# Kernel optimization log

Measured on AMD Instinct MI355X. Metric: run time of the kernel, lower is better.

Reference implementation:

```python
import jax, jax.numpy as jnp
import numpy as np

N = 1024   # state dimension
L = 16384  # sequence length


def setup_inputs() -> dict:
    key = jax.random.key(0)
    k_u, k_a, k_b, k_c = jax.random.split(key, 4)
    u = jax.random.normal(k_u, (L,), dtype=jnp.float32)
    # lecun_normal: std = 1/sqrt(fan_in). Shift A by -I so the discretized
    # transition matrix Ab has spectral radius < 1 (otherwise Ab^L overflows).
    A = jax.random.normal(k_a, (N, N), dtype=jnp.float32) / np.sqrt(N) - jnp.eye(N, dtype=jnp.float32)
    B = jax.random.normal(k_b, (N, 1), dtype=jnp.float32) / np.sqrt(1.0)
    C = jax.random.normal(k_c, (1, N), dtype=jnp.float32) / np.sqrt(N)
    log_step = jnp.full((1, 1), np.log(0.01), dtype=jnp.float32)
    return {"u": u, "A": A, "B": B, "C": C, "log_step": log_step}


def reference(u, A, B, C, log_step):
    # --- discretize (bilinear / Tustin transform) ---
    step = jnp.exp(log_step)[0, 0]
    I = jnp.eye(A.shape[0], dtype=A.dtype)
    BL = jnp.linalg.inv(I - (step / 2.0) * A)
    Ab = BL @ (I + (step / 2.0) * A)     # (N, N)
    Bb = (step * BL) @ B                  # (N, 1)
    Cb = C                                # (1, N)

    # --- naive_kernel: K[l] = Cb @ Ab^l @ Bb, built as a scan recurrence ---
    def body(x, _):
        k_l = (Cb @ x)[0, 0]
        return Ab @ x, k_l

    _, K = jax.lax.scan(body, Bb, None, length=u.shape[0])  # (L,)

    # --- causal convolution: y[t] = sum_{l<=t} K[l] * u[t-l] ---
    y = jnp.convolve(u, K)[: u.shape[0]]
    return y
```

## Files before the change

kernel.cpp:

```cpp
#include <hip/hip_runtime.h>
#include <hip/hip_bf16.h>
#include <math.h>

#define N_DIM 1024
#define L_SEQ 16384

typedef unsigned short ushort_t;
typedef __bf16 bf16x8 __attribute__((ext_vector_type(8)));
typedef float f32x4 __attribute__((ext_vector_type(4)));

#define FW_F32 1
#define FW_SPLIT 2
#define FW_TSPLIT 4
#define FW_ADDD 8
#define FW_MKAB 16
#define FW_TPRE 32

#define AS1 __attribute__((address_space(1)))
#define AS3 __attribute__((address_space(3)))

__device__ __forceinline__ void split2(float v, ushort_t& h, ushort_t& m) {
  union { __bf16 b; ushort_t u; } c;
  __bf16 bh = (__bf16)v;
  float fh = (float)bh;
  c.b = bh; h = c.u;
  c.b = (__bf16)(v - fh); m = c.u;
}

__global__ __launch_bounds__(256) void k_scalesplit(const float* __restrict__ A,
    const float* __restrict__ ls, float* __restrict__ E,
    ushort_t* __restrict__ set) {
  const size_t NN = (size_t)N_DIM * N_DIM;
  float hs = 0.5f * expf(ls[0]);
  int t = threadIdx.x;
  int r0 = blockIdx.x * 64 + ((t >> 4) << 2);
  int c0 = blockIdx.y * 64 + ((t & 15) << 2);
  float v[4][4];
#pragma unroll
  for (int i = 0; i < 4; ++i) {
    float4 f = *(const float4*)&A[(size_t)(r0 + i) * N_DIM + c0];
    v[i][0] = hs * f.x; v[i][1] = hs * f.y; v[i][2] = hs * f.z; v[i][3] = hs * f.w;
    *(float4*)&E[(size_t)(r0 + i) * N_DIM + c0] =
        make_float4(v[i][0], v[i][1], v[i][2], v[i][3]);
  }
  ushort_t h[4][4], m[4][4];
#pragma unroll
  for (int i = 0; i < 4; ++i)
#pragma unroll
    for (int j = 0; j < 4; ++j) split2(v[i][j], h[i][j], m[i][j]);
#pragma unroll
  for (int i = 0; i < 4; ++i) {
    size_t o = (size_t)(r0 + i) * N_DIM + c0;
    *(ushort4*)&set[o] = make_ushort4(h[i][0], h[i][1], h[i][2], h[i][3]);
    *(ushort4*)&set[NN + o] = make_ushort4(m[i][0], m[i][1], m[i][2], m[i][3]);
  }
#pragma unroll
  for (int j = 0; j < 4; ++j) {
    size_t o = (size_t)(c0 + j) * N_DIM + r0;
    *(ushort4*)&set[2 * NN + o] = make_ushort4(h[0][j], h[1][j], h[2][j], h[3][j]);
    *(ushort4*)&set[3 * NN + o] = make_ushort4(m[0][j], m[1][j], m[2][j], m[3][j]);
  }
}

__global__ __launch_bounds__(256) void k_bbinit(ushort_t* __restrict__ VTset,
    ushort_t* __restrict__ Wset, const float* __restrict__ S,
    const float* __restrict__ B, const float* __restrict__ Cm,
    const float* __restrict__ ls) {
  const size_t KR = (size_t)128 * N_DIM;
  int bx = blockIdx.x;
  if (bx >= 256) {
    int i = (bx - 256) * 256 + threadIdx.x;
    ushort_t h, m; split2(Cm[i], h, m);
    Wset[i] = h; Wset[KR + i] = m;
    return;
  }
  int row = bx * 4 + (threadIdx.x >> 6);
  int lane = threadIdx.x & 63;
  const float* Sr = S + (size_t)row * N_DIM;
  float sum = 0.f;
  for (int k = lane; k < N_DIM; k += 64) sum += Sr[k] * B[k];
  for (int off = 32; off; off >>= 1) sum += __shfl_down(sum, off);
  if (lane == 0) {
    float step = expf(ls[0]);
    float bb = step * (B[row] + sum);
    ushort_t h, m; split2(bb, h, m);
    VTset[row] = h; VTset[KR + row] = m;
  }
}

__device__ __forceinline__ void skinny_q(
    ushort_t* lds, const ushort_t* __restrict__ SkB, ushort_t* __restrict__ Ka,
    int srcOff, int dstOff, int cnt, int id, int t) {
  const size_t NN = (size_t)N_DIM * N_DIM;
  const size_t KR = (size_t)128 * N_DIM;
  int rt = id >> 6, c16 = id & 63;
  if (rt * 16 >= cnt) return;
  const int lane = t & 63, w = t >> 6;
  const ushort_t* Ah = Ka;
  const ushort_t* Amm = Ka + KR;
  const ushort_t* Bh = SkB;
  const ushort_t* Bm = SkB + NN;

  auto stq = [&](int buf, int k0) {
    ushort_t* base = lds + buf * 2048;
    if (t < 128) {
      int pl = t >> 6, rem = t & 63, kc = rem >> 4, row = rem & 15;
      const ushort_t* src = (pl ? Amm : Ah) +
          (size_t)(srcOff + rt * 16 + row) * N_DIM + k0 + kc * 8;
      __builtin_amdgcn_global_load_lds((const AS1 void*)src,
                                       (AS3 void*)(base + t * 8), 16, 0, 0);
    } else {
      int t2 = t - 128;
      int pl = t2 >> 6, rem = t2 & 63, kc = rem >> 4, row = rem & 15;
      const ushort_t* src = (pl ? Bm : Bh) +
          (size_t)(c16 * 16 + row) * N_DIM + k0 + kc * 8;
      __builtin_amdgcn_global_load_lds((const AS1 void*)src,
                                       (AS3 void*)(base + 1024 + t2 * 8), 16, 0, 0);
    }
  };

  f32x4 acc = (f32x4){0.f, 0.f, 0.f, 0.f};
  const int lrow = lane & 15, kg = lane >> 4;

  stq(0, 0);
  stq(1, 32);
  for (int ks = 0; ks < 32; ++ks) {
    int cur = ks % 3;
    if (ks < 30) {
      stq((ks + 2) % 3, (ks + 2) * 32);
      asm volatile("s_waitcnt vmcnt(2)" ::: "memory");
    } else if (ks == 30) {
      asm volatile("s_waitcnt vmcnt(1)" ::: "memory");
    } else {
      asm volatile("s_waitcnt vmcnt(0)" ::: "memory");
    }
    __builtin_amdgcn_s_barrier();
    __builtin_amdgcn_sched_barrier(0);
    if (w == 0) {
      const ushort_t* b = lds + cur * 2048;
      bf16x8 a0 = *(const bf16x8*)&b[kg * 128 + lrow * 8];
      bf16x8 a1 = *(const bf16x8*)&b[512 + kg * 128 + lrow * 8];
      bf16x8 b0 = *(const bf16x8*)&b[1024 + kg * 128 + lrow * 8];
      bf16x8 b1 = *(const bf16x8*)&b[1536 + kg * 128 + lrow * 8];
      acc = __builtin_amdgcn_mfma_f32_16x16x32_bf16(a0, b0, acc, 0, 0, 0);
      acc = __builtin_amdgcn_mfma_f32_16x16x32_bf16(a0, b1, acc, 0, 0, 0);
      acc = __builtin_amdgcn_mfma_f32_16x16x32_bf16(a1, b0, acc, 0, 0, 0);
      acc = __builtin_amdgcn_mfma_f32_16x16x32_bf16(a1, b1, acc, 0, 0, 0);
    }
    if (ks < 31) __builtin_amdgcn_s_barrier();
  }

  if (w == 0) {
    int col = c16 * 16 + lrow;
#pragma unroll
    for (int j = 0; j < 4; ++j) {
      int irl = kg * 4 + j;
      if (rt * 16 + irl < cnt) {
        ushort_t h, m; split2(acc[j], h, m);
        Ka[(size_t)(dstOff + rt * 16 + irl) * N_DIM + col] = h;
        Ka[KR + (size_t)(dstOff + rt * 16 + irl) * N_DIM + col] = m;
      }
    }
  }
}

__global__ __launch_bounds__(256) void gemm4f(
    const ushort_t* __restrict__ Qa, const ushort_t* __restrict__ Qbt,
    const float* __restrict__ D, float* __restrict__ Cf,
    ushort_t* __restrict__ Oset, ushort_t* __restrict__ Oset2, int flags,
    const ushort_t* __restrict__ SkB, ushort_t* __restrict__ Ka,
    int srcOff, int dstOff, int cnt, int mode) {
  const size_t NN = (size_t)N_DIM * N_DIM;
  const size_t KR = (size_t)128 * N_DIM;
  __shared__ __align__(16) ushort_t lds[30720];
  int t = threadIdx.x;
  const int lane = t & 63, w = t >> 6;
  int id = (int)blockIdx.y * 16 + (int)blockIdx.x;

  if (mode == 2) {
    skinny_q(lds, SkB, Ka, srcOff, dstOff, cnt, id, t);
    return;
  }

  int m0 = blockIdx.x * 64, n0 = blockIdx.y * 64;
  int r = t & 63, kc = t >> 6;
  const ushort_t* gA[2] = {Qa, Qa + NN};
  const ushort_t* gB[2] = {Qbt, Qbt + NN};
  size_t aoff = (size_t)(m0 + r) * N_DIM + kc * 8;
  size_t boff = (size_t)(n0 + r) * N_DIM + kc * 8;

  int rt = id >> 6, c16 = id & 63;
  bool hasSk = (mode == 1) && (rt * 16 < cnt);
  const ushort_t* skAh = Ka;
  const ushort_t* skAm = Ka + KR;
  const ushort_t* skBh = SkB;
  const ushort_t* skBm = SkB ? SkB + NN : SkB;

  auto stage = [&](int buf, int k0) {
    ushort_t* dst = lds + buf * 8192;
#pragma unroll
    for (int L = 0; L < 2; ++L) {
      __builtin_amdgcn_global_load_lds(
          (const AS1 void*)(gA[L] + aoff + k0),
          (AS3 void*)(dst + L * 2048 + t * 8), 16, 0, 0);
      __builtin_amdgcn_global_load_lds(
          (const AS1 void*)(gB[L] + boff + k0),
          (AS3 void*)(dst + 4096 + L * 2048 + t * 8), 16, 0, 0);
    }
  };
  auto stq = [&](int buf, int k0) {
    ushort_t* base = lds + 24576 + buf * 2048;
    if (t < 128) {
      int pl = t >> 6, rem = t & 63, skc = rem >> 4, row = rem & 15;
      const ushort_t* src = (pl ? skAm : skAh) +
          (size_t)(srcOff + rt * 16 + row) * N_DIM + k0 + skc * 8;
      __builtin_amdgcn_global_load_lds((const AS1 void*)src,
                                       (AS3 void*)(base + t * 8), 16, 0, 0);
    } else {
      int t2 = t - 128;
      int pl = t2 >> 6, rem = t2 & 63, skc = rem >> 4, row = rem & 15;
      const ushort_t* src = (pl ? skBm : skBh) +
          (size_t)(c16 * 16 + row) * N_DIM + k0 + skc * 8;
      __builtin_amdgcn_global_load_lds((const AS1 void*)src,
                                       (AS3 void*)(base + 1024 + t2 * 8), 16, 0, 0);
    }
  };

  f32x4 acc[2][2];
#pragma unroll
  for (int i = 0; i < 2; ++i)
#pragma unroll
    for (int j = 0; j < 2; ++j) acc[i][j] = (f32x4){0.f, 0.f, 0.f, 0.f};
  f32x4 skacc = (f32x4){0.f, 0.f, 0.f, 0.f};

  const int wm = (w >> 1) * 32, wn = (w & 1) * 32;
  const int lrow = lane & 15, kg = lane >> 4;
  const int aIdx0 = kg * 512 + (wm + lrow) * 8;
  const int bIdx0 = 4096 + kg * 512 + (wn + lrow) * 8;

#pragma unroll
  for (int p = 0; p < 2; ++p) {
    stage(p, p * 32);
    if (hasSk) stq(p, p * 32);
  }
  for (int ks = 0; ks < 32; ++ks) {
    int cur = ks % 3;
    if (ks < 30) {
      stage((ks + 2) % 3, (ks + 2) * 32);
      if (hasSk) {
        stq((ks + 2) % 3, (ks + 2) * 32);
        asm volatile("s_waitcnt vmcnt(10)" ::: "memory");
      } else {
        asm volatile("s_waitcnt vmcnt(8)" ::: "memory");
      }
    } else if (ks == 30) {
      if (hasSk) asm volatile("s_waitcnt vmcnt(5)" ::: "memory");
      else       asm volatile("s_waitcnt vmcnt(4)" ::: "memory");
    } else {
      asm volatile("s_waitcnt vmcnt(0)" ::: "memory");
    }
    __builtin_amdgcn_s_barrier();
    __builtin_amdgcn_sched_barrier(0);
    const ushort_t* buf = lds + cur * 8192;
    bf16x8 a[2][2], b[2][2];
#pragma unroll
    for (int L = 0; L < 2; ++L) {
#pragma unroll
      for (int mi = 0; mi < 2; ++mi)
        a[L][mi] = *(const bf16x8*)&buf[L * 2048 + aIdx0 + mi * 128];
#pragma unroll
      for (int ni = 0; ni < 2; ++ni)
        b[L][ni] = *(const bf16x8*)&buf[bIdx0 + L * 2048 + ni * 128];
    }
#pragma unroll
    for (int mi = 0; mi < 2; ++mi)
#pragma unroll
      for (int ni = 0; ni < 2; ++ni) {
        f32x4 c = acc[mi][ni];
        c = __builtin_amdgcn_mfma_f32_16x16x32_bf16(a[0][mi], b[0][ni], c, 0, 0, 0);
        c = __builtin_amdgcn_mfma_f32_16x16x32_bf16(a[0][mi], b[1][ni], c, 0, 0, 0);
        c = __builtin_amdgcn_mfma_f32_16x16x32_bf16(a[1][mi], b[0][ni], c, 0, 0, 0);
        c = __builtin_amdgcn_mfma_f32_16x16x32_bf16(a[1][mi], b[1][ni], c, 0, 0, 0);
        acc[mi][ni] = c;
      }
    if (hasSk && w == 0) {
      const ushort_t* sb = lds + 24576 + cur * 2048;
      bf16x8 sa0 = *(const bf16x8*)&sb[kg * 128 + lrow * 8];
      bf16x8 sa1 = *(const bf16x8*)&sb[512 + kg * 128 + lrow * 8];
      bf16x8 sb0 = *(const bf16x8*)&sb[1024 + kg * 128 + lrow * 8];
      bf16x8 sb1 = *(const bf16x8*)&sb[1536 + kg * 128 + lrow * 8];
      skacc = __builtin_amdgcn_mfma_f32_16x16x32_bf16(sa0, sb0, skacc, 0, 0, 0);
      skacc = __builtin_amdgcn_mfma_f32_16x16x32_bf16(sa0, sb1, skacc, 0, 0, 0);
      skacc = __builtin_amdgcn_mfma_f32_16x16x32_bf16(sa1, sb0, skacc, 0, 0, 0);
      skacc = __builtin_amdgcn_mfma_f32_16x16x32_bf16(sa1, sb1, skacc, 0, 0, 0);
    }
    if (ks < 31) __builtin_amdgcn_s_barrier();
  }

#pragma unroll
  for (int mi = 0; mi < 2; ++mi)
#pragma unroll
    for (int ni = 0; ni < 2; ++ni) {
      int rowb = m0 + wm + mi * 16 + kg * 4;
      int col = n0 + wn + ni * 16 + lrow;
      float vv[4];
#pragma unroll
      for (int j = 0; j < 4; ++j) vv[j] = acc[mi][ni][j];
      if (flags & FW_TPRE) {
        ushort_t h[4], m[4];
#pragma unroll
        for (int j = 0; j < 4; ++j) split2(vv[j], h[j], m[j]);
        size_t o = (size_t)col * N_DIM + rowb;
        *(ushort4*)&Oset2[2 * NN + o] = make_ushort4(h[0], h[1], h[2], h[3]);
        *(ushort4*)&Oset2[3 * NN + o] = make_ushort4(m[0], m[1], m[2], m[3]);
      }
      if (flags & FW_ADDD) {
#pragma unroll
        for (int j = 0; j < 4; ++j) vv[j] += D[(size_t)(rowb + j) * N_DIM + col];
      }
      if (flags & FW_F32) {
#pragma unroll
        for (int j = 0; j < 4; ++j) Cf[(size_t)(rowb + j) * N_DIM + col] = vv[j];
      }
      if (flags & FW_MKAB) {
#pragma unroll
        for (int j = 0; j < 4; ++j)
          vv[j] = 2.0f * vv[j] + ((rowb + j) == col ? 1.0f : 0.0f);
      }
      if (flags & (FW_SPLIT | FW_TSPLIT)) {
        ushort_t h[4], m[4];
#pragma unroll
        for (int j = 0; j < 4; ++j) split2(vv[j], h[j], m[j]);
        if (flags & FW_SPLIT) {
#pragma unroll
          for (int j = 0; j < 4; ++j) {
            size_t o = (size_t)(rowb + j) * N_DIM + col;
            Oset[o] = h[j]; Oset[NN + o] = m[j];
          }
        }
        if (flags & FW_TSPLIT) {
          size_t o = (size_t)col * N_DIM + rowb;
          *(ushort4*)&Oset[2 * NN + o] = make_ushort4(h[0], h[1], h[2], h[3]);
          *(ushort4*)&Oset[3 * NN + o] = make_ushort4(m[0], m[1], m[2], m[3]);
        }
      }
    }

  if (hasSk && w == 0) {
    int col = c16 * 16 + lrow;
#pragma unroll
    for (int j = 0; j < 4; ++j) {
      int irl = kg * 4 + j;
      if (rt * 16 + irl < cnt) {
        ushort_t h, m; split2(skacc[j], h, m);
        Ka[(size_t)(dstOff + rt * 16 + irl) * N_DIM + col] = h;
        Ka[KR + (size_t)(dstOff + rt * 16 + irl) * N_DIM + col] = m;
      }
    }
  }
}

__global__ __launch_bounds__(256) void k_combine(
    const ushort_t* __restrict__ Wset, const ushort_t* __restrict__ Vset,
    float* __restrict__ Kv) {
  const size_t KR = (size_t)128 * N_DIM;
  __shared__ __align__(16) ushort_t lds[15360];
  int t = threadIdx.x;
  int rt = blockIdx.x, ct = blockIdx.y;
  const ushort_t* Ah = Wset;
  const ushort_t* Amm = Wset + KR;
  const ushort_t* Bh = Vset;
  const ushort_t* Bm = Vset + KR;
  const int lane = t & 63, w = t >> 6;
  const int lrow = lane & 15, kg = lane >> 4;

  auto stageS = [&](int buf, int k0) {
    ushort_t* base = lds + buf * 5120;
    if (t < 128) {
      int lvl = t >> 6, rem = t & 63, kcc = rem >> 4, i = rem & 15;
      const ushort_t* src =
          (lvl ? Amm : Ah) + (size_t)(rt * 16 + i) * N_DIM + k0 + kcc * 8;
      __builtin_amdgcn_global_load_lds((const AS1 void*)src,
                                       (AS3 void*)(base + t * 8), 16, 0, 0);
    }
#pragma unroll
    for (int it = 0; it < 2; ++it) {
      int t2 = t + it * 256;
      int lvl = t2 >> 8, rem = t2 & 255, kcc = rem >> 6, c = rem & 63;
      const ushort_t* src =
          (lvl ? Bm : Bh) + (size_t)(ct * 64 + c) * N_DIM + k0 + kcc * 8;
      __builtin_amdgcn_global_load_lds(
          (const AS1 void*)src, (AS3 void*)(base + 1024 + t2 * 8), 16, 0, 0);
    }
  };

  f32x4 acc = (f32x4){0.f, 0.f, 0.f, 0.f};
  const int aO = kg * 128 + lrow * 8;
  const int bO = 1024 + kg * 512 + (w * 16 + lrow) * 8;

  stageS(0, 0);
  stageS(1, 32);
  for (int ks = 0; ks < 32; ++ks) {
    int cur = ks % 3;
    if (ks < 30) {
      stageS((ks + 2) % 3, (ks + 2) * 32);
      if (w < 2) asm volatile("s_waitcnt vmcnt(6)" ::: "memory");
      else       asm volatile("s_waitcnt vmcnt(4)" ::: "memory");
    } else if (ks == 30) {
      if (w < 2) asm volatile("s_waitcnt vmcnt(3)" ::: "memory");
      else       asm volatile("s_waitcnt vmcnt(2)" ::: "memory");
    } else {
      asm volatile("s_waitcnt vmcnt(0)" ::: "memory");
    }
    __builtin_amdgcn_s_barrier();
    __builtin_amdgcn_sched_barrier(0);
    const ushort_t* b = lds + cur * 5120;
    bf16x8 a0 = *(const bf16x8*)&b[aO];
    bf16x8 a1 = *(const bf16x8*)&b[aO + 512];
    bf16x8 b0v = *(const bf16x8*)&b[bO];
    bf16x8 b1v = *(const bf16x8*)&b[bO + 2048];
    acc = __builtin_amdgcn_mfma_f32_16x16x32_bf16(a0, b0v, acc, 0, 0, 0);
    acc = __builtin_amdgcn_mfma_f32_16x16x32_bf16(a0, b1v, acc, 0, 0, 0);
    acc = __builtin_amdgcn_mfma_f32_16x16x32_bf16(a1, b0v, acc, 0, 0, 0);
    acc = __builtin_amdgcn_mfma_f32_16x16x32_bf16(a1, b1v, acc, 0, 0, 0);
    if (ks < 31) __builtin_amdgcn_s_barrier();
  }

  int rcol = ct * 64 + w * 16 + lrow;
#pragma unroll
  for (int j = 0; j < 4; ++j) {
    int q = rt * 16 + kg * 4 + j;
    Kv[q * 128 + rcol] = acc[j];
  }
}

__global__ __launch_bounds__(256) void conv_k(const float* __restrict__ Kv,
    const float* __restrict__ u, float* __restrict__ y) {
  const int CT = 1024, CJ = 256, LCH = 1024;
  int t0 = blockIdx.x * CT;
  int l0 = blockIdx.y * LCH;
  if (l0 > t0 + CT - 1) return;
  __shared__ __align__(16) float Ks[CJ];
  __shared__ __align__(16) float us[CT + CJ + 8];
  int tid = threadIdx.x;
  float acc0 = 0.f, acc1 = 0.f, acc2 = 0.f, acc3 = 0.f;
  int ltEnd = l0 + LCH; if (ltEnd > t0 + CT) ltEnd = t0 + CT;
  for (int lt = l0; lt < ltEnd; lt += CJ) {
    __syncthreads();
    Ks[tid] = Kv[lt + tid];
    int ub = t0 - lt - (CJ - 1);
    for (int s = tid; s < CT + CJ + 4; s += 256) {
      int g = ub + s;
      us[s] = (g >= 0 && g < L_SEQ) ? u[g] : 0.f;
    }
    __syncthreads();
    const float4* u4 = (const float4*)us;
    float4 wa = u4[tid];
#pragma unroll 4
    for (int jb = 0; jb < CJ / 4; ++jb) {
      float4 wb = u4[tid + jb + 1];
      float4 k4 = *(const float4*)&Ks[CJ - 4 - (jb << 2)];
      acc0 += k4.w * wa.x + k4.z * wa.y + k4.y * wa.z + k4.x * wa.w;
      acc1 += k4.w * wa.y + k4.z * wa.z + k4.y * wa.w + k4.x * wb.x;
      acc2 += k4.w * wa.z + k4.z * wa.w + k4.y * wb.x + k4.x * wb.y;
      acc3 += k4.w * wa.w + k4.z * wb.x + k4.y * wb.y + k4.x * wb.z;
      wa = wb;
    }
  }
  int t = t0 + (tid << 2);
  atomicAdd(&y[t + 0], acc0);
  atomicAdd(&y[t + 1], acc1);
  atomicAdd(&y[t + 2], acc2);
  atomicAdd(&y[t + 3], acc3);
}


extern "C" void kernel_launch(void* const* d_in, const int* in_sizes, int n_in,
                              void* d_out, int out_size, void* d_ws, size_t ws_size,
                              hipStream_t stream) {
  const float* u  = (const float*)d_in[0];
  const float* A  = (const float*)d_in[1];
  const float* B  = (const float*)d_in[2];
  const float* Cm = (const float*)d_in[3];
  const float* ls = (const float*)d_in[4];
  float* y  = (float*)d_out;
  float* ws = (float*)d_ws;

  const int N = N_DIM;
  const size_t NN = (size_t)N * N;
  const size_t KR = (size_t)128 * N;
  float* b0 = ws;
  float* b2 = b0 + NN;
  float* Kv = b2 + NN;
  ushort_t* setA = (ushort_t*)(Kv + L_SEQ);
  ushort_t* setB = setA + 4 * NN;
  ushort_t* setC = setB + 4 * NN;
  ushort_t* VTset = setC + 4 * NN;
  ushort_t* Wset = VTset + 2 * KR;

  hipMemsetAsync(y, 0, (size_t)L_SEQ * sizeof(float), stream);

  dim3 g16(16, 16);
  dim3 gQ32(16, 8);

  k_scalesplit<<<g16, 256, 0, stream>>>(A, ls, b0, setA);
  gemm4f<<<g16, 256, 0, stream>>>(setA, setA + 2 * NN, b0, b2, setC, setB,
                                  FW_TPRE | FW_ADDD | FW_F32 | FW_SPLIT,
                                  nullptr, nullptr, 0, 0, 0, 0);
  gemm4f<<<g16, 256, 0, stream>>>(setC, setB + 2 * NN, b2, b0, setA, nullptr,
                                  FW_ADDD | FW_F32 | FW_MKAB | FW_SPLIT | FW_TSPLIT,
                                  nullptr, nullptr, 0, 0, 0, 0);
  k_bbinit<<<260, 256, 0, stream>>>(VTset, Wset, b0, B, Cm, ls);

  ushort_t* cur = setA;
  ushort_t* oth = setB;
  for (int e = 0; e < 12; ++e) {
    int right = (e < 7);
    int s = 1 << (right ? e : (e - 7));
    ushort_t* Ka = right ? VTset : Wset;
    const ushort_t* SkB = right ? cur : cur + 2 * NN;
    int fl = (e == 11) ? FW_TSPLIT : (FW_SPLIT | FW_TSPLIT);
    gemm4f<<<g16, 256, 0, stream>>>(cur, cur + 2 * NN, nullptr, nullptr,
                                    oth, nullptr, fl, SkB, Ka, 0, s, s, 1);
    ushort_t* tmp = cur; cur = oth; oth = tmp;
  }
  const ushort_t* Q12T = cur + 2 * NN;
  for (int p = 0; p < 3; ++p)
    gemm4f<<<gQ32, 256, 0, stream>>>(cur, cur, nullptr, nullptr,
                                     nullptr, nullptr, 0, Q12T, Wset,
                                     32 * p, 32 + 32 * p, 32, 2);
  k_combine<<<dim3(8, 2), 256, 0, stream>>>(Wset, VTset, Kv);
  conv_k<<<g16, 256, 0, stream>>>(Kv, u, y);
}
```

Before: 393.6 us.

## Overlap final combine tiles with skinny Q doubling launches via extra block row

Removes the standalone k_combine kernel and spreads its 16 tiles across the three skinny-Q launches plus a small final launch. Each skinny launch gets an extra grid row whose first four blocks compute the combine tiles for the W rows finished in earlier passes. The aim is to hide combine work behind the skinny GEMM and trim the serial tail. It depends on row chunks of Wset already being complete when they are read. The cost is extra blocks and more kernel parameters.

```diff
diff --git a/kernel.cpp b/kernel.cpp
--- a/kernel.cpp
+++ b/kernel.cpp
@@ -85,6 +85,78 @@
     float bb = step * (B[row] + sum);
     ushort_t h, m; split2(bb, h, m);
     VTset[row] = h; VTset[KR + row] = m;
+  }
+}
+
+__device__ __forceinline__ void combine_tile(
+    ushort_t* lds, const ushort_t* __restrict__ Wset,
+    const ushort_t* __restrict__ Vset, float* __restrict__ Kv,
+    int rt, int ct, int t) {
+  const size_t KR = (size_t)128 * N_DIM;
+  const ushort_t* Ah = Wset;
+  const ushort_t* Amm = Wset + KR;
+  const ushort_t* Bh = Vset;
+  const ushort_t* Bm = Vset + KR;
+  const int lane = t & 63, w = t >> 6;
+  const int lrow = lane & 15, kg = lane >> 4;
+
+  auto stageS = [&](int buf, int k0) {
+    ushort_t* base = lds + buf * 5120;
+    if (t < 128) {
+      int lvl = t >> 6, rem = t & 63, kcc = rem >> 4, i = rem & 15;
+      const ushort_t* src =
+          (lvl ? Amm : Ah) + (size_t)(rt * 16 + i) * N_DIM + k0 + kcc * 8;
+      __builtin_amdgcn_global_load_lds((const AS1 void*)src,
+                                       (AS3 void*)(base + t * 8), 16, 0, 0);
+    }
+#pragma unroll
+    for (int it = 0; it < 2; ++it) {
+      int t2 = t + it * 256;
+      int lvl = t2 >> 8, rem = t2 & 255, kcc = rem >> 6, c = rem & 63;
+      const ushort_t* src =
+          (lvl ? Bm : Bh) + (size_t)(ct * 64 + c) * N_DIM + k0 + kcc * 8;
+      __builtin_amdgcn_global_load_lds(
+          (const AS1 void*)src, (AS3 void*)(base + 1024 + t2 * 8), 16, 0, 0);
+    }
+  };
+
+  f32x4 acc = (f32x4){0.f, 0.f, 0.f, 0.f};
+  const int aO = kg * 128 + lrow * 8;
+  const int bO = 1024 + kg * 512 + (w * 16 + lrow) * 8;
+
+  stageS(0, 0);
+  stageS(1, 32);
+  for (int ks = 0; ks < 32; ++ks) {
+    int cur = ks % 3;
+    if (ks < 30) {
+      stageS((ks + 2) % 3, (ks + 2) * 32);
+      if (w < 2) asm volatile("s_waitcnt vmcnt(6)" ::: "memory");
+      else       asm volatile("s_waitcnt vmcnt(4)" ::: "memory");
+    } else if (ks == 30) {
+      if (w < 2) asm volatile("s_waitcnt vmcnt(3)" ::: "memory");
+      else       asm volatile("s_waitcnt vmcnt(2)" ::: "memory");
+    } else {
+      asm volatile("s_waitcnt vmcnt(0)" ::: "memory");
+    }
+    __builtin_amdgcn_s_barrier();
+    __builtin_amdgcn_sched_barrier(0);
+    const ushort_t* b = lds + cur * 5120;
+    bf16x8 a0 = *(const bf16x8*)&b[aO];
+    bf16x8 a1 = *(const bf16x8*)&b[aO + 512];
+    bf16x8 b0v = *(const bf16x8*)&b[bO];
+    bf16x8 b1v = *(const bf16x8*)&b[bO + 2048];
+    acc = __builtin_amdgcn_mfma_f32_16x16x32_bf16(a0, b0v, acc, 0, 0, 0);
+    acc = __builtin_amdgcn_mfma_f32_16x16x32_bf16(a0, b1v, acc, 0, 0, 0);
+    acc = __builtin_amdgcn_mfma_f32_16x16x32_bf16(a1, b0v, acc, 0, 0, 0);
+    acc = __builtin_amdgcn_mfma_f32_16x16x32_bf16(a1, b1v, acc, 0, 0, 0);
+    if (ks < 31) __builtin_amdgcn_s_barrier();
+  }
+
+  int rcol = ct * 64 + w * 16 + lrow;
+#pragma unroll
+  for (int j = 0; j < 4; ++j) {
+    int q = rt * 16 + kg * 4 + j;
+    Kv[q * 128 + rcol] = acc[j];
   }
 }
 
@@ -169,7 +241,8 @@
     const float* __restrict__ D, float* __restrict__ Cf,
     ushort_t* __restrict__ Oset, ushort_t* __restrict__ Oset2, int flags,
     const ushort_t* __restrict__ SkB, ushort_t* __restrict__ Ka,
-    int srcOff, int dstOff, int cnt, int mode) {
+    int srcOff, int dstOff, int cnt, int mode,
+    const ushort_t* __restrict__ Vt, float* __restrict__ Kv, int chunk) {
   const size_t NN = (size_t)N_DIM * N_DIM;
   const size_t KR = (size_t)128 * N_DIM;
   __shared__ __align__(16) ushort_t lds[30720];
@@ -177,7 +250,18 @@
   const int lane = t & 63, w = t >> 6;
   int id = (int)blockIdx.y * 16 + (int)blockIdx.x;
 
+  if (mode == 3) {
+    combine_tile(lds, Ka, Vt, Kv, 2 * chunk + ((int)blockIdx.x >> 1),
+                 (int)blockIdx.x & 1, t);
+    return;
+  }
   if (mode == 2) {
+    if ((int)blockIdx.y == 8) {
+      if ((int)blockIdx.x < 4 && chunk >= 0)
+        combine_tile(lds, Ka, Vt, Kv, 2 * chunk + ((int)blockIdx.x >> 1),
+                     (int)blockIdx.x & 1, t);
+      return;
+    }
     skinny_q(lds, SkB, Ka, srcOff, dstOff, cnt, id, t);
     return;
   }
@@ -357,80 +441,6 @@
         Ka[KR + (size_t)(dstOff + rt * 16 + irl) * N_DIM + col] = m;
       }
     }
-  }
-}
-
-__global__ __launch_bounds__(256) void k_combine(
-    const ushort_t* __restrict__ Wset, const ushort_t* __restrict__ Vset,
-    float* __restrict__ Kv) {
-  const size_t KR = (size_t)128 * N_DIM;
-  __shared__ __align__(16) ushort_t lds[15360];
-  int t = threadIdx.x;
-  int rt = blockIdx.x, ct = blockIdx.y;
-  const ushort_t* Ah = Wset;
-  const ushort_t* Amm = Wset + KR;
-  const ushort_t* Bh = Vset;
-  const ushort_t* Bm = Vset + KR;
-  const int lane = t & 63, w = t >> 6;
-  const int lrow = lane & 15, kg = lane >> 4;
-
-  auto stageS = [&](int buf, int k0) {
-    ushort_t* base = lds + buf * 5120;
-    if (t < 128) {
-      int lvl = t >> 6, rem = t & 63, kcc = rem >> 4, i = rem & 15;
-      const ushort_t* src =
-          (lvl ? Amm : Ah) + (size_t)(rt * 16 + i) * N_DIM + k0 + kcc * 8;
-      __builtin_amdgcn_global_load_lds((const AS1 void*)src,
-                                       (AS3 void*)(base + t * 8), 16, 0, 0);
-    }
-#pragma unroll
-    for (int it = 0; it < 2; ++it) {
-      int t2 = t + it * 256;
-      int lvl = t2 >> 8, rem = t2 & 255, kcc = rem >> 6, c = rem & 63;
-      const ushort_t* src =
-          (lvl ? Bm : Bh) + (size_t)(ct * 64 + c) * N_DIM + k0 + kcc * 8;
-      __builtin_amdgcn_global_load_lds(
-          (const AS1 void*)src, (AS3 void*)(base + 1024 + t2 * 8), 16, 0, 0);
-    }
-  };
-
-  f32x4 acc = (f32x4){0.f, 0.f, 0.f, 0.f};
-  const int aO = kg * 128 + lrow * 8;
-  const int bO = 1024 + kg * 512 + (w * 16 + lrow) * 8;
-
-  stageS(0, 0);
-  stageS(1, 32);
-  for (int ks = 0; ks < 32; ++ks) {
-    int cur = ks % 3;
-    if (ks < 30) {
-      stageS((ks + 2) % 3, (ks + 2) * 32);
-      if (w < 2) asm volatile("s_waitcnt vmcnt(6)" ::: "memory");
-      else       asm volatile("s_waitcnt vmcnt(4)" ::: "memory");
-    } else if (ks == 30) {
-      if (w < 2) asm volatile("s_waitcnt vmcnt(3)" ::: "memory");
-      else       asm volatile("s_waitcnt vmcnt(2)" ::: "memory");
-    } else {
-      asm volatile("s_waitcnt vmcnt(0)" ::: "memory");
-    }
-    __builtin_amdgcn_s_barrier();
-    __builtin_amdgcn_sched_barrier(0);
-    const ushort_t* b = lds + cur * 5120;
-    bf16x8 a0 = *(const bf16x8*)&b[aO];
-    bf16x8 a1 = *(const bf16x8*)&b[aO + 512];
-    bf16x8 b0v = *(const bf16x8*)&b[bO];
-    bf16x8 b1v = *(const bf16x8*)&b[bO + 2048];
-    acc = __builtin_amdgcn_mfma_f32_16x16x32_bf16(a0, b0v, acc, 0, 0, 0);
-    acc = __builtin_amdgcn_mfma_f32_16x16x32_bf16(a0, b1v, acc, 0, 0, 0);
-    acc = __builtin_amdgcn_mfma_f32_16x16x32_bf16(a1, b0v, acc, 0, 0, 0);
-    acc = __builtin_amdgcn_mfma_f32_16x16x32_bf16(a1, b1v, acc, 0, 0, 0);
-    if (ks < 31) __builtin_amdgcn_s_barrier();
-  }
-
-  int rcol = ct * 64 + w * 16 + lrow;
-#pragma unroll
-  for (int j = 0; j < 4; ++j) {
-    int q = rt * 16 + kg * 4 + j;
-    Kv[q * 128 + rcol] = acc[j];
   }
 }
 
@@ -501,15 +511,18 @@
   hipMemsetAsync(y, 0, (size_t)L_SEQ * sizeof(float), stream);
 
   dim3 g16(16, 16);
-  dim3 gQ32(16, 8);
+  dim3 gQC(16, 9);
+  dim3 gC4(4, 1);
 
   k_scalesplit<<<g16, 256, 0, stream>>>(A, ls, b0, setA);
   gemm4f<<<g16, 256, 0, stream>>>(setA, setA + 2 * NN, b0, b2, setC, setB,
                                   FW_TPRE | FW_ADDD | FW_F32 | FW_SPLIT,
-                                  nullptr, nullptr, 0, 0, 0, 0);
+                                  nullptr, nullptr, 0, 0, 0, 0,
+                                  nullptr, nullptr, -1);
   gemm4f<<<g16, 256, 0, stream>>>(setC, setB + 2 * NN, b2, b0, setA, nullptr,
                                   FW_ADDD | FW_F32 | FW_MKAB | FW_SPLIT | FW_TSPLIT,
-                                  nullptr, nullptr, 0, 0, 0, 0);
+                                  nullptr, nullptr, 0, 0, 0, 0,
+                                  nullptr, nullptr, -1);
   k_bbinit<<<260, 256, 0, stream>>>(VTset, Wset, b0, B, Cm, ls);
 
   ushort_t* cur = setA;
@@ -521,14 +534,18 @@
     const ushort_t* SkB = right ? cur : cur + 2 * NN;
     int fl = (e == 11) ? FW_TSPLIT : (FW_SPLIT | FW_TSPLIT);
     gemm4f<<<g16, 256, 0, stream>>>(cur, cur + 2 * NN, nullptr, nullptr,
-                                    oth, nullptr, fl, SkB, Ka, 0, s, s, 1);
+                                    oth, nullptr, fl, SkB, Ka, 0, s, s, 1,
+                                    nullptr, nullptr, -1);
     ushort_t* tmp = cur; cur = oth; oth = tmp;
   }
   const ushort_t* Q12T = cur + 2 * NN;
   for (int p = 0; p < 3; ++p)
-    gemm4f<<<gQ32, 256, 0, stream>>>(cur, cur, nullptr, nullptr,
-                                     nullptr, nullptr, 0, Q12T, Wset,
-                                     32 * p, 32 + 32 * p, 32, 2);
-  k_combine<<<dim3(8, 2), 256, 0, stream>>>(Wset, VTset, Kv);
+    gemm4f<<<gQC, 256, 0, stream>>>(cur, cur, nullptr, nullptr,
+                                    nullptr, nullptr, 0, Q12T, Wset,
+                                    32 * p, 32 + 32 * p, 32, 2,
+                                    VTset, Kv, p);
+  gemm4f<<<gC4, 256, 0, stream>>>(nullptr, nullptr, nullptr, nullptr,
+                                  nullptr, nullptr, 0, nullptr, Wset,
+                                  0, 0, 0, 3, VTset, Kv, 3);
   conv_k<<<g16, 256, 0, stream>>>(Kv, u, y);
 }
```

Result: slower. 406.5 us (+3.3%).
